# Performance work log

Hardware: AMD Instinct MI355X
Metric: run time of the kernel (lower is better)

Reference implementation:

```python
import jax, jax.numpy as jnp
import numpy as np

B, N, A, T = 65536, 128, 32, 64


def setup_inputs() -> dict:
    key = jax.random.key(0)
    k1, k2, k3, k4 = jax.random.split(key, 4)
    traj = jax.random.normal(k1, (B, N, 3), dtype=jnp.float32)
    ref_x = jax.random.normal(k2, (A, 3), dtype=jnp.float32)
    ref_x = ref_x - jnp.mean(ref_x, axis=0, keepdims=True)  # centered ref, as in __init__
    align_idx = jnp.sort(jax.random.randint(k3, (A,), 0, N)).astype(jnp.int64)
    train_idx = jnp.sort(jax.random.randint(k4, (T,), 0, N)).astype(jnp.int64)
    return {"traj": traj, "ref_x": ref_x, "align_idx": align_idx, "train_idx": train_idx}


def reference(traj, ref_x, align_idx, train_idx):
    # --- Kabsch alignment ---
    sel = traj[:, align_idx, :]                      # [B, A, 3]
    x_c = jnp.mean(sel, axis=1, keepdims=True)       # [B, 1, 3]
    x0 = sel - x_c                                   # centered selection
    # prod = x0^T @ ref_x : [B, 3, 3]
    prod = jnp.einsum('bai,aj->bij', x0, ref_x)
    u, s, vh = jnp.linalg.svd(prod)                  # batched 3x3 SVD
    # proper-rotation sign fix (det of u @ vh), detached in the original
    sign = jax.lax.stop_gradient(jnp.sign(jnp.linalg.det(jnp.matmul(u, vh))))  # [B]
    d = jnp.stack([jnp.ones_like(sign), jnp.ones_like(sign), sign], axis=-1)   # [B, 3]
    rotate = jnp.matmul(u * d[:, None, :], vh)       # u @ diag(1,1,sign) @ vh, [B,3,3]
    aligned = jnp.matmul(traj - x_c, rotate)         # [B, N, 3]
    # --- select train atoms and flatten ---
    out = aligned[:, train_idx, :].reshape(traj.shape[0], -1)  # [B, T*3]
    return out
```

## Files before the change

kernel.cpp:

```cpp
#include <hip/hip_runtime.h>
#include <math.h>

#define N_ATOMS  128
#define A_ALIGN  32
#define T_TRAIN  64
#define ROWF     (N_ATOMS*3)
#define R4       (ROWF/4)

template<int p, int q, int r>
__device__ __forceinline__ void jrot(float Am[3][3], float Vm[3][3])
{
    float apq = Am[p][q];
    float app = Am[p][p];
    float aqq = Am[q][q];
    float tau = (aqq - app) / (2.0f * apq);
    float tt  = 1.0f / (fabsf(tau) + sqrtf(1.0f + tau * tau));
    float t   = copysignf(tt, tau);
    t = (fabsf(apq) > 1e-20f) ? t : 0.0f;
    float c = 1.0f / sqrtf(1.0f + t * t);
    float s = t * c;
    float arp = Am[r][p], arq = Am[r][q];
    float nrp = c * arp - s * arq;
    float nrq = s * arp + c * arq;
    Am[r][p] = nrp; Am[p][r] = nrp;
    Am[r][q] = nrq; Am[q][r] = nrq;
    Am[p][p] = app - t * apq;
    Am[q][q] = aqq + t * apq;
    Am[p][q] = 0.0f; Am[q][p] = 0.0f;
#pragma unroll
    for (int k = 0; k < 3; ++k) {
        float vp = Vm[k][p], vq = Vm[k][q];
        Vm[k][p] = c * vp - s * vq;
        Vm[k][q] = s * vp + c * vq;
    }
}

template<bool FUSED>
__global__ __launch_bounds__(64)
void kabsch_rot_kernel(const float* __restrict__ traj,
                       const float* __restrict__ ref_x,
                       const int*   __restrict__ align_idx,
                       const int*   __restrict__ train_idx,
                       float*       __restrict__ rws,
                       float*       __restrict__ out,
                       int B)
{
    int b = blockIdx.x * 64 + threadIdx.x;
    if (b >= B) return;
    const float* __restrict__ row = traj + (size_t)b * ROWF;

    float S00=0,S01=0,S02=0,S10=0,S11=0,S12=0,S20=0,S21=0,S22=0;
    float xs0=0,xs1=0,xs2=0, rs0=0,rs1=0,rs2=0;
#pragma unroll
    for (int a = 0; a < A_ALIGN; ++a) {
        int ia = align_idx[a];
        float px = row[ia*3+0], py = row[ia*3+1], pz = row[ia*3+2];
        float rx = ref_x[a*3+0], ry = ref_x[a*3+1], rz = ref_x[a*3+2];
        S00 += px*rx; S01 += px*ry; S02 += px*rz;
        S10 += py*rx; S11 += py*ry; S12 += py*rz;
        S20 += pz*rx; S21 += pz*ry; S22 += pz*rz;
        xs0 += px; xs1 += py; xs2 += pz;
        rs0 += rx; rs1 += ry; rs2 += rz;
    }
    const float inv_a = 1.0f / (float)A_ALIGN;
    float c0 = xs0*inv_a, c1 = xs1*inv_a, c2 = xs2*inv_a;
    float P00 = S00 - c0*rs0, P01 = S01 - c0*rs1, P02 = S02 - c0*rs2;
    float P10 = S10 - c1*rs0, P11 = S11 - c1*rs1, P12 = S12 - c1*rs2;
    float P20 = S20 - c2*rs0, P21 = S21 - c2*rs1, P22 = S22 - c2*rs2;

    float Am[3][3], Vm[3][3];
    Am[0][0] = P00*P00 + P10*P10 + P20*P20;
    Am[0][1] = P00*P01 + P10*P11 + P20*P21;
    Am[0][2] = P00*P02 + P10*P12 + P20*P22;
    Am[1][1] = P01*P01 + P11*P11 + P21*P21;
    Am[1][2] = P01*P02 + P11*P12 + P21*P22;
    Am[2][2] = P02*P02 + P12*P12 + P22*P22;
    Am[1][0]=Am[0][1]; Am[2][0]=Am[0][2]; Am[2][1]=Am[1][2];
    Vm[0][0]=1.f; Vm[0][1]=0.f; Vm[0][2]=0.f;
    Vm[1][0]=0.f; Vm[1][1]=1.f; Vm[1][2]=0.f;
    Vm[2][0]=0.f; Vm[2][1]=0.f; Vm[2][2]=1.f;
#pragma unroll
    for (int sw = 0; sw < 6; ++sw) {
        jrot<0,1,2>(Am, Vm);
        jrot<0,2,1>(Am, Vm);
        jrot<1,2,0>(Am, Vm);
    }

    float l0 = Am[0][0], l1 = Am[1][1], l2 = Am[2][2];
    float v0x=Vm[0][0], v0y=Vm[1][0], v0z=Vm[2][0];
    float v1x=Vm[0][1], v1y=Vm[1][1], v1z=Vm[2][1];
    if (l0 < l1) { float t; t=l0;l0=l1;l1=t;
                   t=v0x;v0x=v1x;v1x=t; t=v0y;v0y=v1y;v1y=t; t=v0z;v0z=v1z;v1z=t; }
    { float v2x=Vm[0][2], v2y=Vm[1][2], v2z=Vm[2][2];
      if (l0 < l2) { float t; t=l0;l0=l2;l2=t;
                     t=v0x;v0x=v2x;v2x=t; t=v0y;v0y=v2y;v2y=t; t=v0z;v0z=v2z;v2z=t; }
      if (l1 < l2) { float t; t=l1;l1=l2;l2=t;
                     t=v1x;v1x=v2x;v2x=t; t=v1y;v1y=v2y;v2y=t; t=v1z;v1z=v2z;v2z=t; }
    }
    float v2x = v0y*v1z - v0z*v1y;
    float v2y = v0z*v1x - v0x*v1z;
    float v2z = v0x*v1y - v0y*v1x;
    float w0x = P00*v0x + P01*v0y + P02*v0z;
    float w0y = P10*v0x + P11*v0y + P12*v0z;
    float w0z = P20*v0x + P21*v0y + P22*v0z;
    float i0 = 1.0f / sqrtf(fmaxf(w0x*w0x+w0y*w0y+w0z*w0z, 1e-30f));
    float u0x=w0x*i0, u0y=w0y*i0, u0z=w0z*i0;
    float w1x = P00*v1x + P01*v1y + P02*v1z;
    float w1y = P10*v1x + P11*v1y + P12*v1z;
    float w1z = P20*v1x + P21*v1y + P22*v1z;
    float d01 = u0x*w1x + u0y*w1y + u0z*w1z;
    w1x -= d01*u0x; w1y -= d01*u0y; w1z -= d01*u0z;
    float i1 = 1.0f / sqrtf(fmaxf(w1x*w1x+w1y*w1y+w1z*w1z, 1e-30f));
    float u1x=w1x*i1, u1y=w1y*i1, u1z=w1z*i1;
    float u2x = u0y*u1z - u0z*u1y;
    float u2y = u0z*u1x - u0x*u1z;
    float u2z = u0x*u1y - u0y*u1x;

    float R00 = u0x*v0x + u1x*v1x + u2x*v2x;
    float R01 = u0x*v0y + u1x*v1y + u2x*v2y;
    float R02 = u0x*v0z + u1x*v1z + u2x*v2z;
    float R10 = u0y*v0x + u1y*v1x + u2y*v2x;
    float R11 = u0y*v0y + u1y*v1y + u2y*v2y;
    float R12 = u0y*v0z + u1y*v1z + u2y*v2z;
    float R20 = u0z*v0x + u1z*v1x + u2z*v2x;
    float R21 = u0z*v0y + u1z*v1y + u2z*v2y;
    float R22 = u0z*v0z + u1z*v1z + u2z*v2z;

    if (!FUSED) {
        float4* w4 = (float4*)(rws + (size_t)b * 12);
        w4[0] = make_float4(R00, R01, R02, R10);
        w4[1] = make_float4(R11, R12, R20, R21);
        w4[2] = make_float4(R22, c0,  c1,  c2);
    } else {
        float* o = out + (size_t)b * (T_TRAIN*3);
#pragma unroll
        for (int t = 0; t < T_TRAIN; ++t) {
            int ti = train_idx[t];
            float x0 = row[ti*3+0]-c0, x1 = row[ti*3+1]-c1, x2 = row[ti*3+2]-c2;
            o[t*3+0] = x0*R00 + x1*R10 + x2*R20;
            o[t*3+1] = x0*R01 + x1*R11 + x2*R21;
            o[t*3+2] = x0*R02 + x1*R12 + x2*R22;
        }
    }
}

__global__ __launch_bounds__(256)
void apply_wave_kernel(const float* __restrict__ traj,
                       const int*   __restrict__ train_idx,
                       const float* __restrict__ rws,
                       float*       __restrict__ out,
                       int B)
{
    __shared__ float lds[4][2 * ROWF];

    const int tid = threadIdx.x;
    const int w  = tid >> 6;
    const int l  = tid & 63;
    const int h  = l >> 5;
    const int tp = l & 31;

    const long long pair = (long long)blockIdx.x * 4 + w;
    const long long b    = pair * 2;
    if (b >= B) return;
    const long long brow  = b + h;
    const bool      rowok = (brow < B);

    int ti0 = train_idx[tp];
    int ti1 = train_idx[tp + 32];

    const float4* __restrict__ g4 = (const float4*)traj;
    const long long maxf4 = (long long)B * R4;
    long long fb = b * R4;
    long long i0 = fb + l;        if (i0 >= maxf4) i0 = maxf4 - 1;
    long long i1 = fb + 64 + l;   if (i1 >= maxf4) i1 = maxf4 - 1;
    long long i2 = fb + 128 + l;  if (i2 >= maxf4) i2 = maxf4 - 1;
    float4 v0 = g4[i0];
    float4 v1 = g4[i1];
    float4 v2 = g4[i2];

    const float4* __restrict__ r4 =
        (const float4*)(rws + (rowok ? brow : (long long)(B - 1)) * 12);
    float4 q0 = r4[0], q1 = r4[1], q2 = r4[2];

    float4* s4 = (float4*)lds[w];
    s4[l]       = v0;
    s4[64 + l]  = v1;
    s4[128 + l] = v2;

    const float* __restrict__ rb = &lds[w][h * ROWF];
    float R00=q0.x, R01=q0.y, R02=q0.z, R10=q0.w;
    float R11=q1.x, R12=q1.y, R20=q1.z, R21=q1.w;
    float R22=q2.x, c0=q2.y, c1=q2.z, c2=q2.w;

    if (rowok) {
        {
            float x0 = rb[ti0*3+0]-c0, x1 = rb[ti0*3+1]-c1, x2 = rb[ti0*3+2]-c2;
            float3 y;
            y.x = x0*R00 + x1*R10 + x2*R20;
            y.y = x0*R01 + x1*R11 + x2*R21;
            y.z = x0*R02 + x1*R12 + x2*R22;
            *(float3*)(out + (brow * T_TRAIN + tp) * 3) = y;
        }
        {
            float x0 = rb[ti1*3+0]-c0, x1 = rb[ti1*3+1]-c1, x2 = rb[ti1*3+2]-c2;
            float3 y;
            y.x = x0*R00 + x1*R10 + x2*R20;
            y.y = x0*R01 + x1*R11 + x2*R21;
            y.z = x0*R02 + x1*R12 + x2*R22;
            *(float3*)(out + (brow * T_TRAIN + tp + 32) * 3) = y;
        }
    }
}

extern "C" void kernel_launch(void* const* d_in, const int* in_sizes, int n_in,
                              void* d_out, int out_size, void* d_ws, size_t ws_size,
                              hipStream_t stream)
{
    const float* traj      = (const float*)d_in[0];
    const float* ref_x     = (const float*)d_in[1];
    const int*   align_idx = (const int*)d_in[2];
    const int*   train_idx = (const int*)d_in[3];
    float* out = (float*)d_out;
    int B = in_sizes[0] / (N_ATOMS * 3);

    size_t need = (size_t)12 * (size_t)B * sizeof(float);
    if (ws_size >= need) {
        float* rws = (float*)d_ws;
        int nblk1 = (B + 63) / 64;
        kabsch_rot_kernel<false><<<dim3(nblk1), dim3(64), 0, stream>>>(
            traj, ref_x, align_idx, train_idx, rws, out, B);
        long long pairs = ((long long)B + 1) / 2;
        int nblk2 = (int)((pairs + 3) / 4);
        apply_wave_kernel<<<dim3(nblk2), dim3(256), 0, stream>>>(
            traj, train_idx, rws, out, B);
    } else {
        int nblk1 = (B + 63) / 64;
        kabsch_rot_kernel<true><<<dim3(nblk1), dim3(64), 0, stream>>>(
            traj, ref_x, align_idx, train_idx, nullptr, out, B);
    }
}
```

Before: 51.85 us.

## Split covariance into coalesced wave-cooperative kernel, separate SVD chain kernel

The covariance and centroid step moves into its own kernel. Each wave loads two trajectory rows into LDS with coalesced float4 reads and reduces the 32 aligned-atom products with 32-lane shuffles, replacing the old per-thread strided gathers. A second lightweight kernel reads the 12 stored floats per batch, runs the Jacobi SVD and writes the rotation back in place, and the existing apply kernel then runs. This trades uncoalesced per-thread loads for an extra kernel launch, an extra workspace round trip, and a second full read of traj in the apply pass.

Result: slower. 65.98 us (+27.2%).

```diff
diff --git a/kernel.cpp b/kernel.cpp
--- a/kernel.cpp
+++ b/kernel.cpp
@@ -35,38 +35,84 @@
     }
 }
 
-template<bool FUSED>
+__device__ __forceinline__ float redu32(float v)
+{
+#pragma unroll
+    for (int m = 16; m >= 1; m >>= 1)
+        v += __shfl_xor(v, m, 32);
+    return v;
+}
+
+__global__ __launch_bounds__(256)
+void cov_kernel(const float* __restrict__ traj,
+                const float* __restrict__ ref_x,
+                const int*   __restrict__ align_idx,
+                float*       __restrict__ pws,
+                int B)
+{
+    __shared__ float lds[4][2 * ROWF];
+
+    const int tid = threadIdx.x;
+    const int w  = tid >> 6;
+    const int l  = tid & 63;
+    const int h  = l >> 5;
+    const int tp = l & 31;
+
+    const long long pair = (long long)blockIdx.x * 4 + w;
+    const long long b    = pair * 2;
+    if (b >= B) return;
+    const long long brow  = b + h;
+    const bool      rowok = (brow < B);
+
+    int   ia = align_idx[tp];
+    float rx = ref_x[tp*3+0], ry = ref_x[tp*3+1], rz = ref_x[tp*3+2];
+
+    const float4* __restrict__ g4 = (const float4*)traj;
+    const long long maxf4 = (long long)B * R4;
+    long long fb = b * R4;
+    long long i0 = fb + l;        if (i0 >= maxf4) i0 = maxf4 - 1;
+    long long i1 = fb + 64 + l;   if (i1 >= maxf4) i1 = maxf4 - 1;
+    long long i2 = fb + 128 + l;  if (i2 >= maxf4) i2 = maxf4 - 1;
+    float4 v0 = g4[i0];
+    float4 v1 = g4[i1];
+    float4 v2 = g4[i2];
+    float4* s4 = (float4*)lds[w];
+    s4[l]       = v0;
+    s4[64 + l]  = v1;
+    s4[128 + l] = v2;
+
+    const float* __restrict__ rb = &lds[w][h * ROWF];
+    float px = rb[ia*3+0], py = rb[ia*3+1], pz = rb[ia*3+2];
+
+    float S00 = redu32(px*rx), S01 = redu32(px*ry), S02 = redu32(px*rz);
+    float S10 = redu32(py*rx), S11 = redu32(py*ry), S12 = redu32(py*rz);
+    float S20 = redu32(pz*rx), S21 = redu32(pz*ry), S22 = redu32(pz*rz);
+    float xs0 = redu32(px), xs1 = redu32(py), xs2 = redu32(pz);
+    float rs0 = redu32(rx), rs1 = redu32(ry), rs2 = redu32(rz);
+
+    if (tp == 0 && rowok) {
+        const float inv_a = 1.0f / (float)A_ALIGN;
+        float c0 = xs0*inv_a, c1 = xs1*inv_a, c2 = xs2*inv_a;
+        float4* o4 = (float4*)(pws + (size_t)brow * 12);
+        o4[0] = make_float4(S00 - c0*rs0, S01 - c0*rs1, S02 - c0*rs2,
+                            S10 - c1*rs0);
+        o4[1] = make_float4(S11 - c1*rs1, S12 - c1*rs2, S20 - c2*rs0,
+                            S21 - c2*rs1);
+        o4[2] = make_float4(S22 - c2*rs2, c0, c1, c2);
+    }
+}
+
 __global__ __launch_bounds__(64)
-void kabsch_rot_kernel(const float* __restrict__ traj,
-                       const float* __restrict__ ref_x,
-                       const int*   __restrict__ align_idx,
-                       const int*   __restrict__ train_idx,
-                       float*       __restrict__ rws,
-                       float*       __restrict__ out,
-                       int B)
+void chain_kernel(float* __restrict__ pws, int B)
 {
     int b = blockIdx.x * 64 + threadIdx.x;
     if (b >= B) return;
-    const float* __restrict__ row = traj + (size_t)b * ROWF;
-
-    float S00=0,S01=0,S02=0,S10=0,S11=0,S12=0,S20=0,S21=0,S22=0;
-    float xs0=0,xs1=0,xs2=0, rs0=0,rs1=0,rs2=0;
-#pragma unroll
-    for (int a = 0; a < A_ALIGN; ++a) {
-        int ia = align_idx[a];
-        float px = row[ia*3+0], py = row[ia*3+1], pz = row[ia*3+2];
-        float rx = ref_x[a*3+0], ry = ref_x[a*3+1], rz = ref_x[a*3+2];
-        S00 += px*rx; S01 += px*ry; S02 += px*rz;
-        S10 += py*rx; S11 += py*ry; S12 += py*rz;
-        S20 += pz*rx; S21 += pz*ry; S22 += pz*rz;
-        xs0 += px; xs1 += py; xs2 += pz;
-        rs0 += rx; rs1 += ry; rs2 += rz;
-    }
-    const float inv_a = 1.0f / (float)A_ALIGN;
-    float c0 = xs0*inv_a, c1 = xs1*inv_a, c2 = xs2*inv_a;
-    float P00 = S00 - c0*rs0, P01 = S01 - c0*rs1, P02 = S02 - c0*rs2;
-    float P10 = S10 - c1*rs0, P11 = S11 - c1*rs1, P12 = S12 - c1*rs2;
-    float P20 = S20 - c2*rs0, P21 = S21 - c2*rs1, P22 = S22 - c2*rs2;
+
+    float4* w4 = (float4*)(pws + (size_t)b * 12);
+    float4 q0 = w4[0], q1 = w4[1], q2 = w4[2];
+    float P00=q0.x, P01=q0.y, P02=q0.z, P10=q0.w;
+    float P11=q1.x, P12=q1.y, P20=q1.z, P21=q1.w;
+    float P22=q2.x, c0=q2.y, c1=q2.z, c2=q2.w;
 
     float Am[3][3], Vm[3][3];
     Am[0][0] = P00*P00 + P10*P10 + P20*P20;
@@ -116,32 +162,15 @@
     float u2y = u0z*u1x - u0x*u1z;
     float u2z = u0x*u1y - u0y*u1x;
 
-    float R00 = u0x*v0x + u1x*v1x + u2x*v2x;
-    float R01 = u0x*v0y + u1x*v1y + u2x*v2y;
-    float R02 = u0x*v0z + u1x*v1z + u2x*v2z;
-    float R10 = u0y*v0x + u1y*v1x + u2y*v2x;
-    float R11 = u0y*v0y + u1y*v1y + u2y*v2y;
-    float R12 = u0y*v0z + u1y*v1z + u2y*v2z;
-    float R20 = u0z*v0x + u1z*v1x + u2z*v2x;
-    float R21 = u0z*v0y + u1z*v1y + u2z*v2y;
-    float R22 = u0z*v0z + u1z*v1z + u2z*v2z;
-
-    if (!FUSED) {
-        float4* w4 = (float4*)(rws + (size_t)b * 12);
-        w4[0] = make_float4(R00, R01, R02, R10);
-        w4[1] = make_float4(R11, R12, R20, R21);
-        w4[2] = make_float4(R22, c0,  c1,  c2);
-    } else {
-        float* o = out + (size_t)b * (T_TRAIN*3);
-#pragma unroll
-        for (int t = 0; t < T_TRAIN; ++t) {
-            int ti = train_idx[t];
-            float x0 = row[ti*3+0]-c0, x1 = row[ti*3+1]-c1, x2 = row[ti*3+2]-c2;
-            o[t*3+0] = x0*R00 + x1*R10 + x2*R20;
-            o[t*3+1] = x0*R01 + x1*R11 + x2*R21;
-            o[t*3+2] = x0*R02 + x1*R12 + x2*R22;
-        }
-    }
+    w4[0] = make_float4(u0x*v0x + u1x*v1x + u2x*v2x,
+                        u0x*v0y + u1x*v1y + u2x*v2y,
+                        u0x*v0z + u1x*v1z + u2x*v2z,
+                        u0y*v0x + u1y*v1x + u2y*v2x);
+    w4[1] = make_float4(u0y*v0y + u1y*v1y + u2y*v2y,
+                        u0y*v0z + u1y*v1z + u2y*v2z,
+                        u0z*v0x + u1z*v1x + u2z*v2x,
+                        u0z*v0y + u1z*v1y + u2z*v2y);
+    w4[2] = make_float4(u0z*v0z + u1z*v1z + u2z*v2z, c0, c1, c2);
 }
 
 __global__ __launch_bounds__(256)
@@ -212,6 +241,103 @@
     }
 }
 
+__global__ __launch_bounds__(64)
+void kabsch_fused_fallback(const float* __restrict__ traj,
+                           const float* __restrict__ ref_x,
+                           const int*   __restrict__ align_idx,
+                           const int*   __restrict__ train_idx,
+                           float*       __restrict__ out,
+                           int B)
+{
+    int b = blockIdx.x * 64 + threadIdx.x;
+    if (b >= B) return;
+    const float* __restrict__ row = traj + (size_t)b * ROWF;
+
+    float S00=0,S01=0,S02=0,S10=0,S11=0,S12=0,S20=0,S21=0,S22=0;
+    float xs0=0,xs1=0,xs2=0, rs0=0,rs1=0,rs2=0;
+#pragma unroll
+    for (int a = 0; a < A_ALIGN; ++a) {
+        int ia = align_idx[a];
+        float px = row[ia*3+0], py = row[ia*3+1], pz = row[ia*3+2];
+        float rx = ref_x[a*3+0], ry = ref_x[a*3+1], rz = ref_x[a*3+2];
+        S00 += px*rx; S01 += px*ry; S02 += px*rz;
+        S10 += py*rx; S11 += py*ry; S12 += py*rz;
+        S20 += pz*rx; S21 += pz*ry; S22 += pz*rz;
+        xs0 += px; xs1 += py; xs2 += pz;
+        rs0 += rx; rs1 += ry; rs2 += rz;
+    }
+    const float inv_a = 1.0f / (float)A_ALIGN;
+    float c0 = xs0*inv_a, c1 = xs1*inv_a, c2 = xs2*inv_a;
+    float P00 = S00 - c0*rs0, P01 = S01 - c0*rs1, P02 = S02 - c0*rs2;
+    float P10 = S10 - c1*rs0, P11 = S11 - c1*rs1, P12 = S12 - c1*rs2;
+    float P20 = S20 - c2*rs0, P21 = S21 - c2*rs1, P22 = S22 - c2*rs2;
+
+    float Am[3][3], Vm[3][3];
+    Am[0][0] = P00*P00 + P10*P10 + P20*P20;
+    Am[0][1] = P00*P01 + P10*P11 + P20*P21;
+    Am[0][2] = P00*P02 + P10*P12 + P20*P22;
+    Am[1][1] = P01*P01 + P11*P11 + P21*P21;
+    Am[1][2] = P01*P02 + P11*P12 + P21*P22;
+    Am[2][2] = P02*P02 + P12*P12 + P22*P22;
+    Am[1][0]=Am[0][1]; Am[2][0]=Am[0][2]; Am[2][1]=Am[1][2];
+    Vm[0][0]=1.f; Vm[0][1]=0.f; Vm[0][2]=0.f;
+    Vm[1][0]=0.f; Vm[1][1]=1.f; Vm[1][2]=0.f;
+    Vm[2][0]=0.f; Vm[2][1]=0.f; Vm[2][2]=1.f;
+#pragma unroll
+    for (int sw = 0; sw < 6; ++sw) {
+        jrot<0,1,2>(Am, Vm);
+        jrot<0,2,1>(Am, Vm);
+        jrot<1,2,0>(Am, Vm);
+    }
+    float l0 = Am[0][0], l1 = Am[1][1], l2 = Am[2][2];
+    float v0x=Vm[0][0], v0y=Vm[1][0], v0z=Vm[2][0];
+    float v1x=Vm[0][1], v1y=Vm[1][1], v1z=Vm[2][1];
+    if (l0 < l1) { float t; t=l0;l0=l1;l1=t;
+                   t=v0x;v0x=v1x;v1x=t; t=v0y;v0y=v1y;v1y=t; t=v0z;v0z=v1z;v1z=t; }
+    { float v2x=Vm[0][2], v2y=Vm[1][2], v2z=Vm[2][2];
+      if (l0 < l2) { float t; t=l0;l0=l2;l2=t;
+                     t=v0x;v0x=v2x;v2x=t; t=v0y;v0y=v2y;v2y=t; t=v0z;v0z=v2z;v2z=t; }
+      if (l1 < l2) { float t; t=l1;l1=l2;l2=t;
+                     t=v1x;v1x=v2x;v2x=t; t=v1y;v1y=v2y;v2y=t; t=v1z;v1z=v2z;v2z=t; }
+    }
+    float v2x = v0y*v1z - v0z*v1y;
+    float v2y = v0z*v1x - v0x*v1z;
+    float v2z = v0x*v1y - v0y*v1x;
+    float w0x = P00*v0x + P01*v0y + P02*v0z;
+    float w0y = P10*v0x + P11*v0y + P12*v0z;
+    float w0z = P20*v0x + P21*v0y + P22*v0z;
+    float i0 = 1.0f / sqrtf(fmaxf(w0x*w0x+w0y*w0y+w0z*w0z, 1e-30f));
+    float u0x=w0x*i0, u0y=w0y*i0, u0z=w0z*i0;
+    float w1x = P00*v1x + P01*v1y + P02*v1z;
+    float w1y = P10*v1x + P11*v1y + P12*v1z;
+    float w1z = P20*v1x + P21*v1y + P22*v1z;
+    float d01 = u0x*w1x + u0y*w1y + u0z*w1z;
+    w1x -= d01*u0x; w1y -= d01*u0y; w1z -= d01*u0z;
+    float i1 = 1.0f / sqrtf(fmaxf(w1x*w1x+w1y*w1y+w1z*w1z, 1e-30f));
+    float u1x=w1x*i1, u1y=w1y*i1, u1z=w1z*i1;
+    float u2x = u0y*u1z - u0z*u1y;
+    float u2y = u0z*u1x - u0x*u1z;
+    float u2z = u0x*u1y - u0y*u1x;
+    float R00 = u0x*v0x + u1x*v1x + u2x*v2x;
+    float R01 = u0x*v0y + u1x*v1y + u2x*v2y;
+    float R02 = u0x*v0z + u1x*v1z + u2x*v2z;
+    float R10 = u0y*v0x + u1y*v1x + u2y*v2x;
+    float R11 = u0y*v0y + u1y*v1y + u2y*v2y;
+    float R12 = u0y*v0z + u1y*v1z + u2y*v2z;
+    float R20 = u0z*v0x + u1z*v1x + u2z*v2x;
+    float R21 = u0z*v0y + u1z*v1y + u2z*v2y;
+    float R22 = u0z*v0z + u1z*v1z + u2z*v2z;
+    float* o = out + (size_t)b * (T_TRAIN*3);
+#pragma unroll
+    for (int t = 0; t < T_TRAIN; ++t) {
+        int ti = train_idx[t];
+        float x0 = row[ti*3+0]-c0, x1 = row[ti*3+1]-c1, x2 = row[ti*3+2]-c2;
+        o[t*3+0] = x0*R00 + x1*R10 + x2*R20;
+        o[t*3+1] = x0*R01 + x1*R11 + x2*R21;
+        o[t*3+2] = x0*R02 + x1*R12 + x2*R22;
+    }
+}
+
 extern "C" void kernel_launch(void* const* d_in, const int* in_sizes, int n_in,
                               void* d_out, int out_size, void* d_ws, size_t ws_size,
                               hipStream_t stream)
@@ -225,17 +351,18 @@
 
     size_t need = (size_t)12 * (size_t)B * sizeof(float);
     if (ws_size >= need) {
-        float* rws = (float*)d_ws;
-        int nblk1 = (B + 63) / 64;
-        kabsch_rot_kernel<false><<<dim3(nblk1), dim3(64), 0, stream>>>(
-            traj, ref_x, align_idx, train_idx, rws, out, B);
+        float* ws = (float*)d_ws;
         long long pairs = ((long long)B + 1) / 2;
-        int nblk2 = (int)((pairs + 3) / 4);
-        apply_wave_kernel<<<dim3(nblk2), dim3(256), 0, stream>>>(
-            traj, train_idx, rws, out, B);
+        int nblkA = (int)((pairs + 3) / 4);
+        cov_kernel<<<dim3(nblkA), dim3(256), 0, stream>>>(
+            traj, ref_x, align_idx, ws, B);
+        int nblkB = (B + 63) / 64;
+        chain_kernel<<<dim3(nblkB), dim3(64), 0, stream>>>(ws, B);
+        apply_wave_kernel<<<dim3(nblkA), dim3(256), 0, stream>>>(
+            traj, train_idx, ws, out, B);
     } else {
         int nblk1 = (B + 63) / 64;
-        kabsch_rot_kernel<true><<<dim3(nblk1), dim3(64), 0, stream>>>(
-            traj, ref_x, align_idx, train_idx, nullptr, out, B);
-    }
-}
+        kabsch_fused_fallback<<<dim3(nblk1), dim3(64), 0, stream>>>(
+            traj, ref_x, align_idx, train_idx, out, B);
+    }
+}
```

## Fuse Kabsch covariance, SVD and apply into a single block-cooperative kernel

Applied to the files above, without the earlier changes.

Replaces the two-kernel pipeline (per-thread rotation kernel writing to a workspace, then a wave-wide apply kernel) with one kernel in which each 256-thread block handles 64 batch rows. Each wave loads row pairs coalesced into LDS and builds the 3x3 cross-covariance with 32-lane shuffle reductions. One wave then runs the Jacobi SVD for all 64 rows from shared memory, and the waves reload the rows to apply the rotation. This removes the strided per-thread gather of alignment atoms, the workspace round trip and a second launch. In exchange it reads each row twice, relying on cache hits, adds many shuffle reductions, and leaves three waves idle while the SVD runs.

Result: no change. 52.05 us (+0.4%).

```diff
diff --git a/kernel.cpp b/kernel.cpp
--- a/kernel.cpp
+++ b/kernel.cpp
@@ -6,6 +6,8 @@
 #define T_TRAIN  64
 #define ROWF     (N_ATOMS*3)
 #define R4       (ROWF/4)
+#define BPBLK    64
+#define PPW      8
 
 template<int p, int q, int r>
 __device__ __forceinline__ void jrot(float Am[3][3], float Vm[3][3])
@@ -35,123 +37,24 @@
     }
 }
 
-template<bool FUSED>
-__global__ __launch_bounds__(64)
-void kabsch_rot_kernel(const float* __restrict__ traj,
-                       const float* __restrict__ ref_x,
-                       const int*   __restrict__ align_idx,
-                       const int*   __restrict__ train_idx,
-                       float*       __restrict__ rws,
-                       float*       __restrict__ out,
-                       int B)
-{
-    int b = blockIdx.x * 64 + threadIdx.x;
-    if (b >= B) return;
-    const float* __restrict__ row = traj + (size_t)b * ROWF;
-
-    float S00=0,S01=0,S02=0,S10=0,S11=0,S12=0,S20=0,S21=0,S22=0;
-    float xs0=0,xs1=0,xs2=0, rs0=0,rs1=0,rs2=0;
+__device__ __forceinline__ float redu32(float v)
+{
 #pragma unroll
-    for (int a = 0; a < A_ALIGN; ++a) {
-        int ia = align_idx[a];
-        float px = row[ia*3+0], py = row[ia*3+1], pz = row[ia*3+2];
-        float rx = ref_x[a*3+0], ry = ref_x[a*3+1], rz = ref_x[a*3+2];
-        S00 += px*rx; S01 += px*ry; S02 += px*rz;
-        S10 += py*rx; S11 += py*ry; S12 += py*rz;
-        S20 += pz*rx; S21 += pz*ry; S22 += pz*rz;
-        xs0 += px; xs1 += py; xs2 += pz;
-        rs0 += rx; rs1 += ry; rs2 += rz;
-    }
-    const float inv_a = 1.0f / (float)A_ALIGN;
-    float c0 = xs0*inv_a, c1 = xs1*inv_a, c2 = xs2*inv_a;
-    float P00 = S00 - c0*rs0, P01 = S01 - c0*rs1, P02 = S02 - c0*rs2;
-    float P10 = S10 - c1*rs0, P11 = S11 - c1*rs1, P12 = S12 - c1*rs2;
-    float P20 = S20 - c2*rs0, P21 = S21 - c2*rs1, P22 = S22 - c2*rs2;
-
-    float Am[3][3], Vm[3][3];
-    Am[0][0] = P00*P00 + P10*P10 + P20*P20;
-    Am[0][1] = P00*P01 + P10*P11 + P20*P21;
-    Am[0][2] = P00*P02 + P10*P12 + P20*P22;
-    Am[1][1] = P01*P01 + P11*P11 + P21*P21;
-    Am[1][2] = P01*P02 + P11*P12 + P21*P22;
-    Am[2][2] = P02*P02 + P12*P12 + P22*P22;
-    Am[1][0]=Am[0][1]; Am[2][0]=Am[0][2]; Am[2][1]=Am[1][2];
-    Vm[0][0]=1.f; Vm[0][1]=0.f; Vm[0][2]=0.f;
-    Vm[1][0]=0.f; Vm[1][1]=1.f; Vm[1][2]=0.f;
-    Vm[2][0]=0.f; Vm[2][1]=0.f; Vm[2][2]=1.f;
-#pragma unroll
-    for (int sw = 0; sw < 6; ++sw) {
-        jrot<0,1,2>(Am, Vm);
-        jrot<0,2,1>(Am, Vm);
-        jrot<1,2,0>(Am, Vm);
-    }
-
-    float l0 = Am[0][0], l1 = Am[1][1], l2 = Am[2][2];
-    float v0x=Vm[0][0], v0y=Vm[1][0], v0z=Vm[2][0];
-    float v1x=Vm[0][1], v1y=Vm[1][1], v1z=Vm[2][1];
-    if (l0 < l1) { float t; t=l0;l0=l1;l1=t;
-                   t=v0x;v0x=v1x;v1x=t; t=v0y;v0y=v1y;v1y=t; t=v0z;v0z=v1z;v1z=t; }
-    { float v2x=Vm[0][2], v2y=Vm[1][2], v2z=Vm[2][2];
-      if (l0 < l2) { float t; t=l0;l0=l2;l2=t;
-                     t=v0x;v0x=v2x;v2x=t; t=v0y;v0y=v2y;v2y=t; t=v0z;v0z=v2z;v2z=t; }
-      if (l1 < l2) { float t; t=l1;l1=l2;l2=t;
-                     t=v1x;v1x=v2x;v2x=t; t=v1y;v1y=v2y;v2y=t; t=v1z;v1z=v2z;v2z=t; }
-    }
-    float v2x = v0y*v1z - v0z*v1y;
-    float v2y = v0z*v1x - v0x*v1z;
-    float v2z = v0x*v1y - v0y*v1x;
-    float w0x = P00*v0x + P01*v0y + P02*v0z;
-    float w0y = P10*v0x + P11*v0y + P12*v0z;
-    float w0z = P20*v0x + P21*v0y + P22*v0z;
-    float i0 = 1.0f / sqrtf(fmaxf(w0x*w0x+w0y*w0y+w0z*w0z, 1e-30f));
-    float u0x=w0x*i0, u0y=w0y*i0, u0z=w0z*i0;
-    float w1x = P00*v1x + P01*v1y + P02*v1z;
-    float w1y = P10*v1x + P11*v1y + P12*v1z;
-    float w1z = P20*v1x + P21*v1y + P22*v1z;
-    float d01 = u0x*w1x + u0y*w1y + u0z*w1z;
-    w1x -= d01*u0x; w1y -= d01*u0y; w1z -= d01*u0z;
-    float i1 = 1.0f / sqrtf(fmaxf(w1x*w1x+w1y*w1y+w1z*w1z, 1e-30f));
-    float u1x=w1x*i1, u1y=w1y*i1, u1z=w1z*i1;
-    float u2x = u0y*u1z - u0z*u1y;
-    float u2y = u0z*u1x - u0x*u1z;
-    float u2z = u0x*u1y - u0y*u1x;
-
-    float R00 = u0x*v0x + u1x*v1x + u2x*v2x;
-    float R01 = u0x*v0y + u1x*v1y + u2x*v2y;
-    float R02 = u0x*v0z + u1x*v1z + u2x*v2z;
-    float R10 = u0y*v0x + u1y*v1x + u2y*v2x;
-    float R11 = u0y*v0y + u1y*v1y + u2y*v2y;
-    float R12 = u0y*v0z + u1y*v1z + u2y*v2z;
-    float R20 = u0z*v0x + u1z*v1x + u2z*v2x;
-    float R21 = u0z*v0y + u1z*v1y + u2z*v2y;
-    float R22 = u0z*v0z + u1z*v1z + u2z*v2z;
-
-    if (!FUSED) {
-        float4* w4 = (float4*)(rws + (size_t)b * 12);
-        w4[0] = make_float4(R00, R01, R02, R10);
-        w4[1] = make_float4(R11, R12, R20, R21);
-        w4[2] = make_float4(R22, c0,  c1,  c2);
-    } else {
-        float* o = out + (size_t)b * (T_TRAIN*3);
-#pragma unroll
-        for (int t = 0; t < T_TRAIN; ++t) {
-            int ti = train_idx[t];
-            float x0 = row[ti*3+0]-c0, x1 = row[ti*3+1]-c1, x2 = row[ti*3+2]-c2;
-            o[t*3+0] = x0*R00 + x1*R10 + x2*R20;
-            o[t*3+1] = x0*R01 + x1*R11 + x2*R21;
-            o[t*3+2] = x0*R02 + x1*R12 + x2*R22;
-        }
-    }
+    for (int m = 16; m >= 1; m >>= 1)
+        v += __shfl_xor(v, m, 32);
+    return v;
 }
 
 __global__ __launch_bounds__(256)
-void apply_wave_kernel(const float* __restrict__ traj,
-                       const int*   __restrict__ train_idx,
-                       const float* __restrict__ rws,
-                       float*       __restrict__ out,
-                       int B)
-{
-    __shared__ float lds[4][2 * ROWF];
+void kabsch_onepass_kernel(const float* __restrict__ traj,
+                           const float* __restrict__ ref_x,
+                           const int*   __restrict__ align_idx,
+                           const int*   __restrict__ train_idx,
+                           float*       __restrict__ out,
+                           int B)
+{
+    __shared__ float slice[4][2 * ROWF];
+    __shared__ float Pbuf[BPBLK][12];
 
     const int tid = threadIdx.x;
     const int w  = tid >> 6;
@@ -159,55 +62,163 @@
     const int h  = l >> 5;
     const int tp = l & 31;
 
-    const long long pair = (long long)blockIdx.x * 4 + w;
-    const long long b    = pair * 2;
-    if (b >= B) return;
-    const long long brow  = b + h;
-    const bool      rowok = (brow < B);
-
-    int ti0 = train_idx[tp];
-    int ti1 = train_idx[tp + 32];
+    const long long bbase = (long long)blockIdx.x * BPBLK;
+
+    const int   ia = align_idx[tp];
+    const float rx = ref_x[tp*3+0], ry = ref_x[tp*3+1], rz = ref_x[tp*3+2];
+    const int   ti0 = train_idx[tp];
+    const int   ti1 = train_idx[tp + 32];
 
     const float4* __restrict__ g4 = (const float4*)traj;
     const long long maxf4 = (long long)B * R4;
-    long long fb = b * R4;
-    long long i0 = fb + l;        if (i0 >= maxf4) i0 = maxf4 - 1;
-    long long i1 = fb + 64 + l;   if (i1 >= maxf4) i1 = maxf4 - 1;
-    long long i2 = fb + 128 + l;  if (i2 >= maxf4) i2 = maxf4 - 1;
-    float4 v0 = g4[i0];
-    float4 v1 = g4[i1];
-    float4 v2 = g4[i2];
-
-    const float4* __restrict__ r4 =
-        (const float4*)(rws + (rowok ? brow : (long long)(B - 1)) * 12);
-    float4 q0 = r4[0], q1 = r4[1], q2 = r4[2];
-
-    float4* s4 = (float4*)lds[w];
-    s4[l]       = v0;
-    s4[64 + l]  = v1;
-    s4[128 + l] = v2;
-
-    const float* __restrict__ rb = &lds[w][h * ROWF];
-    float R00=q0.x, R01=q0.y, R02=q0.z, R10=q0.w;
-    float R11=q1.x, R12=q1.y, R20=q1.z, R21=q1.w;
-    float R22=q2.x, c0=q2.y, c1=q2.z, c2=q2.w;
-
-    if (rowok) {
-        {
-            float x0 = rb[ti0*3+0]-c0, x1 = rb[ti0*3+1]-c1, x2 = rb[ti0*3+2]-c2;
-            float3 y;
-            y.x = x0*R00 + x1*R10 + x2*R20;
-            y.y = x0*R01 + x1*R11 + x2*R21;
-            y.z = x0*R02 + x1*R12 + x2*R22;
-            *(float3*)(out + (brow * T_TRAIN + tp) * 3) = y;
-        }
-        {
-            float x0 = rb[ti1*3+0]-c0, x1 = rb[ti1*3+1]-c1, x2 = rb[ti1*3+2]-c2;
-            float3 y;
-            y.x = x0*R00 + x1*R10 + x2*R20;
-            y.y = x0*R01 + x1*R11 + x2*R21;
-            y.z = x0*R02 + x1*R12 + x2*R22;
-            *(float3*)(out + (brow * T_TRAIN + tp + 32) * 3) = y;
+    float4* s4 = (float4*)slice[w];
+    const float* __restrict__ rb = &slice[w][h * ROWF];
+
+#pragma unroll 1
+    for (int it = 0; it < PPW; ++it) {
+        int pl = w * PPW + it;
+        long long b = bbase + (long long)pl * 2;
+        if (b >= B) break;
+        long long fb = b * R4;
+        long long i0 = fb + l;        if (i0 >= maxf4) i0 = maxf4 - 1;
+        long long i1 = fb + 64 + l;   if (i1 >= maxf4) i1 = maxf4 - 1;
+        long long i2 = fb + 128 + l;  if (i2 >= maxf4) i2 = maxf4 - 1;
+        float4 v0 = g4[i0];
+        float4 v1 = g4[i1];
+        float4 v2 = g4[i2];
+        s4[l]       = v0;
+        s4[64 + l]  = v1;
+        s4[128 + l] = v2;
+
+        float px = rb[ia*3+0], py = rb[ia*3+1], pz = rb[ia*3+2];
+
+        float S00 = redu32(px*rx), S01 = redu32(px*ry), S02 = redu32(px*rz);
+        float S10 = redu32(py*rx), S11 = redu32(py*ry), S12 = redu32(py*rz);
+        float S20 = redu32(pz*rx), S21 = redu32(pz*ry), S22 = redu32(pz*rz);
+        float xs0 = redu32(px), xs1 = redu32(py), xs2 = redu32(pz);
+        float rs0 = redu32(rx), rs1 = redu32(ry), rs2 = redu32(rz);
+
+        if (tp == 0 && (b + h) < B) {
+            const float inv_a = 1.0f / (float)A_ALIGN;
+            float c0 = xs0*inv_a, c1 = xs1*inv_a, c2 = xs2*inv_a;
+            float4* o4 = (float4*)Pbuf[pl*2 + h];
+            o4[0] = make_float4(S00 - c0*rs0, S01 - c0*rs1, S02 - c0*rs2,
+                                S10 - c1*rs0);
+            o4[1] = make_float4(S11 - c1*rs1, S12 - c1*rs2, S20 - c2*rs0,
+                                S21 - c2*rs1);
+            o4[2] = make_float4(S22 - c2*rs2, c0, c1, c2);
+        }
+    }
+    __syncthreads();
+
+    const int cw = blockIdx.x & 3;
+    if ((tid >> 6) == cw && (bbase + (tid & 63)) < B) {
+        const int r = tid & 63;
+        float4* w4 = (float4*)Pbuf[r];
+        float4 q0 = w4[0], q1 = w4[1], q2 = w4[2];
+        float P00=q0.x, P01=q0.y, P02=q0.z, P10=q0.w;
+        float P11=q1.x, P12=q1.y, P20=q1.z, P21=q1.w;
+        float P22=q2.x, c0=q2.y, c1=q2.z, c2=q2.w;
+
+        float Am[3][3], Vm[3][3];
+        Am[0][0] = P00*P00 + P10*P10 + P20*P20;
+        Am[0][1] = P00*P01 + P10*P11 + P20*P21;
+        Am[0][2] = P00*P02 + P10*P12 + P20*P22;
+        Am[1][1] = P01*P01 + P11*P11 + P21*P21;
+        Am[1][2] = P01*P02 + P11*P12 + P21*P22;
+        Am[2][2] = P02*P02 + P12*P12 + P22*P22;
+        Am[1][0]=Am[0][1]; Am[2][0]=Am[0][2]; Am[2][1]=Am[1][2];
+        Vm[0][0]=1.f; Vm[0][1]=0.f; Vm[0][2]=0.f;
+        Vm[1][0]=0.f; Vm[1][1]=1.f; Vm[1][2]=0.f;
+        Vm[2][0]=0.f; Vm[2][1]=0.f; Vm[2][2]=1.f;
+#pragma unroll
+        for (int sw = 0; sw < 6; ++sw) {
+            jrot<0,1,2>(Am, Vm);
+            jrot<0,2,1>(Am, Vm);
+            jrot<1,2,0>(Am, Vm);
+        }
+
+        float l0 = Am[0][0], l1 = Am[1][1], l2 = Am[2][2];
+        float v0x=Vm[0][0], v0y=Vm[1][0], v0z=Vm[2][0];
+        float v1x=Vm[0][1], v1y=Vm[1][1], v1z=Vm[2][1];
+        if (l0 < l1) { float t; t=l0;l0=l1;l1=t;
+                       t=v0x;v0x=v1x;v1x=t; t=v0y;v0y=v1y;v1y=t; t=v0z;v0z=v1z;v1z=t; }
+        { float v2x=Vm[0][2], v2y=Vm[1][2], v2z=Vm[2][2];
+          if (l0 < l2) { float t; t=l0;l0=l2;l2=t;
+                         t=v0x;v0x=v2x;v2x=t; t=v0y;v0y=v2y;v2y=t; t=v0z;v0z=v2z;v2z=t; }
+          if (l1 < l2) { float t; t=l1;l1=l2;l2=t;
+                         t=v1x;v1x=v2x;v2x=t; t=v1y;v1y=v2y;v2y=t; t=v1z;v1z=v2z;v2z=t; }
+        }
+        float v2x = v0y*v1z - v0z*v1y;
+        float v2y = v0z*v1x - v0x*v1z;
+        float v2z = v0x*v1y - v0y*v1x;
+        float w0x = P00*v0x + P01*v0y + P02*v0z;
+        float w0y = P10*v0x + P11*v0y + P12*v0z;
+        float w0z = P20*v0x + P21*v0y + P22*v0z;
+        float i0 = 1.0f / sqrtf(fmaxf(w0x*w0x+w0y*w0y+w0z*w0z, 1e-30f));
+        float u0x=w0x*i0, u0y=w0y*i0, u0z=w0z*i0;
+        float w1x = P00*v1x + P01*v1y + P02*v1z;
+        float w1y = P10*v1x + P11*v1y + P12*v1z;
+        float w1z = P20*v1x + P21*v1y + P22*v1z;
+        float d01 = u0x*w1x + u0y*w1y + u0z*w1z;
+        w1x -= d01*u0x; w1y -= d01*u0y; w1z -= d01*u0z;
+        float i1 = 1.0f / sqrtf(fmaxf(w1x*w1x+w1y*w1y+w1z*w1z, 1e-30f));
+        float u1x=w1x*i1, u1y=w1y*i1, u1z=w1z*i1;
+        float u2x = u0y*u1z - u0z*u1y;
+        float u2y = u0z*u1x - u0x*u1z;
+        float u2z = u0x*u1y - u0y*u1x;
+
+        w4[0] = make_float4(u0x*v0x + u1x*v1x + u2x*v2x,
+                            u0x*v0y + u1x*v1y + u2x*v2y,
+                            u0x*v0z + u1x*v1z + u2x*v2z,
+                            u0y*v0x + u1y*v1x + u2y*v2x);
+        w4[1] = make_float4(u0y*v0y + u1y*v1y + u2y*v2y,
+                            u0y*v0z + u1y*v1z + u2y*v2z,
+                            u0z*v0x + u1z*v1x + u2z*v2x,
+                            u0z*v0y + u1z*v1y + u2z*v2y);
+        w4[2] = make_float4(u0z*v0z + u1z*v1z + u2z*v2z, c0, c1, c2);
+    }
+    __syncthreads();
+
+#pragma unroll 1
+    for (int it = 0; it < PPW; ++it) {
+        int pl = w * PPW + it;
+        long long b = bbase + (long long)pl * 2;
+        if (b >= B) break;
+        long long fb = b * R4;
+        long long i0 = fb + l;        if (i0 >= maxf4) i0 = maxf4 - 1;
+        long long i1 = fb + 64 + l;   if (i1 >= maxf4) i1 = maxf4 - 1;
+        long long i2 = fb + 128 + l;  if (i2 >= maxf4) i2 = maxf4 - 1;
+        float4 v0 = g4[i0];
+        float4 v1 = g4[i1];
+        float4 v2 = g4[i2];
+        s4[l]       = v0;
+        s4[64 + l]  = v1;
+        s4[128 + l] = v2;
+
+        const long long brow = b + h;
+        if (brow < B) {
+            const float4* r4 = (const float4*)Pbuf[pl*2 + h];
+            float4 q0 = r4[0], q1 = r4[1], q2 = r4[2];
+            float R00=q0.x, R01=q0.y, R02=q0.z, R10=q0.w;
+            float R11=q1.x, R12=q1.y, R20=q1.z, R21=q1.w;
+            float R22=q2.x, c0=q2.y, c1=q2.z, c2=q2.w;
+            {
+                float x0 = rb[ti0*3+0]-c0, x1 = rb[ti0*3+1]-c1, x2 = rb[ti0*3+2]-c2;
+                float3 y;
+                y.x = x0*R00 + x1*R10 + x2*R20;
+                y.y = x0*R01 + x1*R11 + x2*R21;
+                y.z = x0*R02 + x1*R12 + x2*R22;
+                *(float3*)(out + (brow * T_TRAIN + ti0*0 + tp) * 3) = y;
+            }
+            {
+                float x0 = rb[ti1*3+0]-c0, x1 = rb[ti1*3+1]-c1, x2 = rb[ti1*3+2]-c2;
+                float3 y;
+                y.x = x0*R00 + x1*R10 + x2*R20;
+                y.y = x0*R01 + x1*R11 + x2*R21;
+                y.z = x0*R02 + x1*R12 + x2*R22;
+                *(float3*)(out + (brow * T_TRAIN + tp + 32) * 3) = y;
+            }
         }
     }
 }
@@ -223,19 +234,7 @@
     float* out = (float*)d_out;
     int B = in_sizes[0] / (N_ATOMS * 3);
 
-    size_t need = (size_t)12 * (size_t)B * sizeof(float);
-    if (ws_size >= need) {
-        float* rws = (float*)d_ws;
-        int nblk1 = (B + 63) / 64;
-        kabsch_rot_kernel<false><<<dim3(nblk1), dim3(64), 0, stream>>>(
-            traj, ref_x, align_idx, train_idx, rws, out, B);
-        long long pairs = ((long long)B + 1) / 2;
-        int nblk2 = (int)((pairs + 3) / 4);
-        apply_wave_kernel<<<dim3(nblk2), dim3(256), 0, stream>>>(
-            traj, train_idx, rws, out, B);
-    } else {
-        int nblk1 = (B + 63) / 64;
-        kabsch_rot_kernel<true><<<dim3(nblk1), dim3(64), 0, stream>>>(
-            traj, ref_x, align_idx, train_idx, nullptr, out, B);
-    }
-}
+    int nblk = (B + BPBLK - 1) / BPBLK;
+    kabsch_onepass_kernel<<<dim3(nblk), dim3(256), 0, stream>>>(
+        traj, ref_x, align_idx, train_idx, out, B);
+}
```
